# Optimization experiments

Measured on AMD Instinct MI355X. Metric: run time of the kernel, lower is better.

Reference implementation:

```python
import jax, jax.numpy as jnp
import numpy as np

N = 100000      # nodes
E = 1600000     # edges
G = 256         # graphs in the batch
D_IN = 128
H = 128
C = 10
EPS = 1e-5      # BatchNorm eps


def setup_inputs() -> dict:
    key = jax.random.key(0)
    ks = jax.random.split(key, 32)
    inp = {
        'x': jax.random.normal(ks[0], (N, D_IN), jnp.float32),
        'edge_index': jax.random.randint(ks[1], (2, E), 0, N, dtype=jnp.int64),
        'batch': jnp.sort(jax.random.randint(ks[2], (N,), 0, G, dtype=jnp.int64)),
        'w1': jax.random.normal(ks[3], (D_IN, H), jnp.float32) * 0.05,
        'b1': jax.random.normal(ks[4], (H,), jnp.float32) * 0.05,
        'w2': jax.random.normal(ks[5], (H, H), jnp.float32) * 0.05,
        'b2': jax.random.normal(ks[6], (H,), jnp.float32) * 0.05,
        'w3': jax.random.normal(ks[7], (H, H), jnp.float32) * 0.05,
        'b3': jax.random.normal(ks[8], (H,), jnp.float32) * 0.05,
        'g1': jax.random.uniform(ks[9], (H,), jnp.float32, 0.5, 1.5),
        'be1': jax.random.normal(ks[10], (H,), jnp.float32) * 0.05,
        'm1': jax.random.normal(ks[11], (H,), jnp.float32) * 0.05,
        'v1': jax.random.uniform(ks[12], (H,), jnp.float32, 0.5, 1.5),
        'g2': jax.random.uniform(ks[13], (H,), jnp.float32, 0.5, 1.5),
        'be2': jax.random.normal(ks[14], (H,), jnp.float32) * 0.05,
        'm2': jax.random.normal(ks[15], (H,), jnp.float32) * 0.05,
        'v2': jax.random.uniform(ks[16], (H,), jnp.float32, 0.5, 1.5),
        'g3': jax.random.uniform(ks[17], (H,), jnp.float32, 0.5, 1.5),
        'be3': jax.random.normal(ks[18], (H,), jnp.float32) * 0.05,
        'm3': jax.random.normal(ks[19], (H,), jnp.float32) * 0.05,
        'v3': jax.random.uniform(ks[20], (H,), jnp.float32, 0.5, 1.5),
        'fcw1': jax.random.normal(ks[21], (H, H // 2), jnp.float32) * 0.05,
        'fcb1': jax.random.normal(ks[22], (H // 2,), jnp.float32) * 0.05,
        'fcw2': jax.random.normal(ks[23], (H // 2, C), jnp.float32) * 0.05,
        'fcb2': jax.random.normal(ks[24], (C,), jnp.float32) * 0.05,
    }
    return inp


def _gcn_norm(edge_index, n_nodes):
    # add self loops (PyG GCNConv default) and compute D^-1/2 (A+I) D^-1/2 norms
    loop = jnp.arange(n_nodes, dtype=edge_index.dtype)
    src = jnp.concatenate([edge_index[0], loop])
    dst = jnp.concatenate([edge_index[1], loop])
    deg = jax.ops.segment_sum(jnp.ones_like(dst, dtype=jnp.float32), dst, num_segments=n_nodes)
    dinv = jnp.where(deg > 0, jax.lax.rsqrt(deg), 0.0)
    norm = dinv[src] * dinv[dst]  # [E+N]
    return src, dst, norm


def _gcn_conv(x, W, b, src, dst, norm, n_nodes):
    h = x @ W                                   # [N, H]
    msg = norm[:, None] * h[src]                # gather + scale, [E+N, H]
    return jax.ops.segment_sum(msg, dst, num_segments=n_nodes) + b


def _bn_eval(x, gamma, beta, mean, var):
    return (x - mean) * jax.lax.rsqrt(var + EPS) * gamma + beta


def reference(x, edge_index, batch, w1, b1, w2, b2, w3, b3,
              g1, be1, m1, v1, g2, be2, m2, v2, g3, be3, m3, v3,
              fcw1, fcb1, fcw2, fcb2):
    n = x.shape[0]
    x = jnp.nan_to_num(x, nan=0.0, posinf=1e6, neginf=-1e6)
    src, dst, norm = _gcn_norm(edge_index, n)

    h = jax.nn.relu(_bn_eval(_gcn_conv(x, w1, b1, src, dst, norm, n), g1, be1, m1, v1))
    h = jax.nn.relu(_bn_eval(_gcn_conv(h, w2, b2, src, dst, norm, n), g2, be2, m2, v2))
    h = jax.nn.relu(_bn_eval(_gcn_conv(h, w3, b3, src, dst, norm, n), g3, be3, m3, v3))

    # global_mean_pool over graphs
    sums = jax.ops.segment_sum(h, batch, num_segments=G)            # [G, H]
    cnts = jax.ops.segment_sum(jnp.ones((n,), h.dtype), batch, num_segments=G)
    pooled = sums / jnp.maximum(cnts, 1.0)[:, None]

    out = jax.nn.relu(pooled @ fcw1 + fcb1) @ fcw2 + fcb2           # [G, C]
    return out
```

## Files before the change

### kernel.cpp

```cpp
#include <hip/hip_runtime.h>
#include <math.h>

#define NN 100000
#define EE 1600000
#define GG 256
#define HH 128
#define BSH 8
#define NBK 391
#define PASSA_WG 391
#define CAPB 6144

typedef __attribute__((ext_vector_type(8))) short short8;
typedef __attribute__((ext_vector_type(4))) float f32x4;

union U4S8 { uint4 u; short8 s; };

static __device__ __forceinline__ unsigned bf16rne(float f) {
    const unsigned u = __float_as_uint(f);
    return (u + 0x7fffu + ((u >> 16) & 1u)) >> 16;
}
static __device__ __forceinline__ unsigned packbf(float a, float b) {
    return bf16rne(a) | (bf16rne(b) << 16);
}
static __device__ __forceinline__ float bflo(unsigned u) { return __uint_as_float(u << 16); }
static __device__ __forceinline__ float bfhi(unsigned u) { return __uint_as_float(u & 0xffff0000u); }

__global__ __launch_bounds__(256) void setup_k(
    const int* __restrict__ ei, const int* __restrict__ batch,
    const float* __restrict__ w1, const float* __restrict__ w2,
    const float* __restrict__ w3,
    const float* __restrict__ b1, const float* __restrict__ g1,
    const float* __restrict__ be1, const float* __restrict__ m1,
    const float* __restrict__ v1,
    const float* __restrict__ b2, const float* __restrict__ g2,
    const float* __restrict__ be2, const float* __restrict__ m2,
    const float* __restrict__ v2,
    const float* __restrict__ b3, const float* __restrict__ g3,
    const float* __restrict__ be3, const float* __restrict__ m3,
    const float* __restrict__ v3,
    unsigned* __restrict__ bt, float* __restrict__ sc, float* __restrict__ sh,
    int* __restrict__ cursor, float* __restrict__ psum, int* __restrict__ gcnt,
    int* __restrict__ flags) {
    const int id = blockIdx.x * 256 + threadIdx.x;
    if (id < 24576) {
        const int w = id >> 13;
        const int rem = id & 8191;
        const int n = rem >> 6;
        const int kk = rem & 63;
        const float* W = (w == 0) ? w1 : (w == 1) ? w2 : w3;
        bt[id] = packbf(W[(2 * kk) * HH + n], W[(2 * kk + 1) * HH + n]);
    } else if (id < 24704) {
        const int c = id - 24576;
        float s;
        s = g1[c] / sqrtf(v1[c] + 1e-5f);
        sc[c] = s;           sh[c] = (b1[c] - m1[c]) * s + be1[c];
        s = g2[c] / sqrtf(v2[c] + 1e-5f);
        sc[128 + c] = s;     sh[128 + c] = (b2[c] - m2[c]) * s + be2[c];
        s = g3[c] / sqrtf(v3[c] + 1e-5f);
        sc[256 + c] = s;     sh[256 + c] = (b3[c] - m3[c]) * s + be3[c];
    } else if (id < 25095) {
        const int b = id - 24704;
        cursor[b] = b * CAPB;
    } else if (id < 57863) {
        psum[id - 25095] = 0.0f;
    } else if (id < 58119) {
        gcnt[id - 57863] = 0;
    } else if (id == 58119) {
        int e64 = 1;
        for (int j = 0; j < 8; ++j) {
            if (ei[2 * EE - 1 - 2 * j] != 0) { e64 = 0; break; }
        }
        flags[0] = e64;
        flags[1] = (batch[NN - 1] == 0) ? 1 : 0;
    }
}
#define SETUP_GRID 228

__global__ __launch_bounds__(256) void passA_k(const int* __restrict__ ei,
                                               const int* __restrict__ flags,
                                               int* __restrict__ cursor,
                                               unsigned* __restrict__ pairs) {
    __shared__ int h[NBK];
    __shared__ int rbase[NBK];
    const int tid = threadIdx.x;
    for (int i = tid; i < NBK; i += 256) h[i] = 0;
    __syncthreads();
    const bool e64 = flags[0] != 0;
    const int base = blockIdx.x * 4096;
    int scache[16], dcache[16];
#pragma unroll
    for (int j = 0; j < 16; ++j) {
        const int e = base + j * 256 + tid;
        int s = -1, d = 0;
        if (e < EE) {
            s = e64 ? ei[2 * e] : ei[e];
            d = e64 ? ei[2 * (EE + e)] : ei[EE + e];
            atomicAdd(&h[d >> BSH], 1);
        }
        scache[j] = s; dcache[j] = d;
    }
    __syncthreads();
    for (int i = tid; i < NBK; i += 256) {
        const int c = h[i];
        rbase[i] = c ? atomicAdd(&cursor[i], c) : 0;
    }
    __syncthreads();
    for (int i = tid; i < NBK; i += 256) h[i] = 0;
    __syncthreads();
#pragma unroll
    for (int j = 0; j < 16; ++j) {
        const int s = scache[j];
        if (s >= 0) {
            const int d = dcache[j];
            const int b = d >> BSH;
            const int r = atomicAdd(&h[b], 1);
            pairs[rbase[b] + r] = ((unsigned)(d & 255) << 17) | (unsigned)s;
        }
    }
}

__global__ __launch_bounds__(256) void passB_k(const unsigned* __restrict__ pairs,
                                               const int* __restrict__ cursor,
                                               int* __restrict__ offs,
                                               int* __restrict__ degcnt,
                                               float* __restrict__ dinv,
                                               int* __restrict__ csr) {
    __shared__ unsigned pk[CAPB];
    __shared__ int cnt[256];
    __shared__ int loff[256];
    __shared__ int sc[256];
    const int tid = threadIdx.x;
    const int b = blockIdx.x;
    const int p0 = b * CAPB;
    const int np = cursor[b] - p0;
    const int nb0 = b << BSH;
    const int nnode = (NN - nb0 < 256) ? (NN - nb0) : 256;

    cnt[tid] = 0;
    __syncthreads();
    for (int i = tid; i < np; i += 256) {
        const unsigned p = pairs[p0 + i];
        pk[i] = p;
        atomicAdd(&cnt[p >> 17], 1);
    }
    __syncthreads();
    const int creal = cnt[tid];
    const int cpad = (tid < nnode) ? ((creal + 8) & ~7) : 0;
    sc[tid] = cpad;
    __syncthreads();
    for (int off = 1; off < 256; off <<= 1) {
        int t = (tid >= off) ? sc[tid - off] : 0;
        __syncthreads();
        sc[tid] += t;
        __syncthreads();
    }
    const int ex = sc[tid] - cpad;
    loff[tid] = ex;
    if (tid < nnode) {
        const int node = nb0 + tid;
        offs[node] = p0 + ex;
        degcnt[node] = creal;
        dinv[node] = 1.0f / sqrtf((float)(creal + 1));
    }
    __syncthreads();
    cnt[tid] = 0;
    __syncthreads();
    for (int i = tid; i < np; i += 256) {
        const unsigned p = pk[i];
        const int dl = (int)(p >> 17);
        const int r = atomicAdd(&cnt[dl], 1);
        csr[p0 + loff[dl] + r] = (int)(p & 0x1FFFFu);
    }
    if (tid < nnode) {
        const int basep = p0 + loff[tid];
        csr[basep + creal] = nb0 + tid;
        for (int j = creal + 1; j < cpad; ++j) csr[basep + j] = NN;
    }
}

static __device__ __forceinline__ float sani(float v) {
    if (isnan(v)) return 0.0f;
    if (isinf(v)) return v > 0.0f ? 1e6f : -1e6f;
    return v;
}

__global__ __launch_bounds__(256) void gemm_mfma_k(const float* __restrict__ Af,
                                                   const unsigned* __restrict__ btg,
                                                   const float* __restrict__ dinv,
                                                   unsigned* __restrict__ C, int M) {
    __shared__ unsigned lds_u[8704];
    const int tid = threadIdx.x;
    const int wave = tid >> 6;
    const int lane = tid & 63;
    const int nl = lane & 15;
    const int q = lane >> 4;
    const int row0 = blockIdx.x * 64 + wave * 16;
    const int rowg = row0 + nl;
    const int rowa = min(rowg, M - 1);

    {
        const uint4* __restrict__ bg4 = (const uint4*)btg;
        for (int i = tid; i < 2048; i += 256) {
            const int n = i >> 4, w4 = i & 15;
            *(uint4*)&lds_u[n * 68 + w4 * 4] = bg4[n * 16 + w4];
        }
    }

    short8 a[4];
#pragma unroll
    for (int ks = 0; ks < 4; ++ks) {
        const float4 p = *(const float4*)(Af + (size_t)rowa * HH + ks * 32 + q * 8);
        const float4 r = *(const float4*)(Af + (size_t)rowa * HH + ks * 32 + q * 8 + 4);
        U4S8 cv;
        cv.u = make_uint4(packbf(sani(p.x), sani(p.y)), packbf(sani(p.z), sani(p.w)),
                          packbf(sani(r.x), sani(r.y)), packbf(sani(r.z), sani(r.w)));
        a[ks] = cv.s;
    }

    __syncthreads();

    f32x4 acc[8];
#pragma unroll
    for (int t = 0; t < 8; ++t) acc[t] = (f32x4)0.0f;

    const unsigned short* __restrict__ bts = (const unsigned short*)lds_u;
#pragma unroll
    for (int ks = 0; ks < 4; ++ks) {
#pragma unroll
        for (int t = 0; t < 8; ++t) {
            const int n = t * 16 + nl;
            const short8 b = *(const short8*)(bts + n * 136 + ks * 32 + q * 8);
            acc[t] = __builtin_amdgcn_mfma_f32_16x16x32_bf16(b, a[ks], acc[t], 0, 0, 0);
        }
    }

    if (rowg < M) {
        const float dsc = dinv[rowg];
        unsigned* crow = C + (size_t)rowg * 64;
#pragma unroll
        for (int t = 0; t < 8; ++t) {
            uint2 o;
            o.x = packbf(dsc * acc[t][0], dsc * acc[t][1]);
            o.y = packbf(dsc * acc[t][2], dsc * acc[t][3]);
            *(uint2*)(crow + t * 8 + q * 2) = o;
        }
    } else if (rowg == M) {
        unsigned* crow = C + (size_t)M * 64;
#pragma unroll
        for (int t = 0; t < 8; ++t)
            *(uint2*)(crow + t * 8 + q * 2) = make_uint2(0u, 0u);
    }
}

__global__ __launch_bounds__(256) void agg_gemm_k(
    const unsigned* __restrict__ hin, const int* __restrict__ csr,
    const int* __restrict__ offs, const int* __restrict__ cnt,
    const float* __restrict__ dinv,
    const float* __restrict__ bnsc, const float* __restrict__ bnsh,
    const unsigned* __restrict__ btg,
    unsigned* __restrict__ hout) {
    __shared__ unsigned ybuf[16 * 68];
    const int tid = threadIdx.x;
    const int wave = tid >> 6;
    const int lane = tid & 63;
    const int cg = lane & 15;
    const int sub = lane >> 4;
    const int c8 = cg * 8;
    const char* __restrict__ hb = (const char*)hin;
    const unsigned cgo = (unsigned)(cg << 4);

    if (blockIdx.x == 0 && tid < 64) hout[(size_t)NN * 64 + tid] = 0u;

    const float4 sca = *(const float4*)(bnsc + c8);
    const float4 scb = *(const float4*)(bnsc + c8 + 4);
    const float4 sha = *(const float4*)(bnsh + c8);
    const float4 shb = *(const float4*)(bnsh + c8 + 4);

    for (int i = 0; i < 4; ++i) {
        const int v = __builtin_amdgcn_readfirstlane(blockIdx.x * 16 + wave * 4 + i);
        const float dv = dinv[v];
        const int start = offs[v];
        const int npad = (cnt[v] + 8) & ~7;

        float acc[8];
#pragma unroll
        for (int j = 0; j < 8; ++j) acc[j] = 0.0f;

        int e = 0;
        for (; e + 16 <= npad; e += 16) {
            const int sA = csr[start + e + sub];
            const int sB = csr[start + e + 4 + sub];
            const int sC = csr[start + e + 8 + sub];
            const int sD = csr[start + e + 12 + sub];
            const uint4 rA = *(const uint4*)(hb + (((unsigned)sA << 8) | cgo));
            const uint4 rB = *(const uint4*)(hb + (((unsigned)sB << 8) | cgo));
            const uint4 rC = *(const uint4*)(hb + (((unsigned)sC << 8) | cgo));
            const uint4 rD = *(const uint4*)(hb + (((unsigned)sD << 8) | cgo));
            acc[0] += (bflo(rA.x) + bflo(rB.x)) + (bflo(rC.x) + bflo(rD.x));
            acc[1] += (bfhi(rA.x) + bfhi(rB.x)) + (bfhi(rC.x) + bfhi(rD.x));
            acc[2] += (bflo(rA.y) + bflo(rB.y)) + (bflo(rC.y) + bflo(rD.y));
            acc[3] += (bfhi(rA.y) + bfhi(rB.y)) + (bfhi(rC.y) + bfhi(rD.y));
            acc[4] += (bflo(rA.z) + bflo(rB.z)) + (bflo(rC.z) + bflo(rD.z));
            acc[5] += (bfhi(rA.z) + bfhi(rB.z)) + (bfhi(rC.z) + bfhi(rD.z));
            acc[6] += (bflo(rA.w) + bflo(rB.w)) + (bflo(rC.w) + bflo(rD.w));
            acc[7] += (bfhi(rA.w) + bfhi(rB.w)) + (bfhi(rC.w) + bfhi(rD.w));
        }
        if (e < npad) {
            const int sA = csr[start + e + sub];
            const int sB = csr[start + e + 4 + sub];
            const uint4 rA = *(const uint4*)(hb + (((unsigned)sA << 8) | cgo));
            const uint4 rB = *(const uint4*)(hb + (((unsigned)sB << 8) | cgo));
            acc[0] += bflo(rA.x) + bflo(rB.x);
            acc[1] += bfhi(rA.x) + bfhi(rB.x);
            acc[2] += bflo(rA.y) + bflo(rB.y);
            acc[3] += bfhi(rA.y) + bfhi(rB.y);
            acc[4] += bflo(rA.z) + bflo(rB.z);
            acc[5] += bfhi(rA.z) + bfhi(rB.z);
            acc[6] += bflo(rA.w) + bflo(rB.w);
            acc[7] += bfhi(rA.w) + bfhi(rB.w);
        }

#pragma unroll
        for (int j = 0; j < 8; ++j) {
            acc[j] += __shfl_xor(acc[j], 16);
            acc[j] += __shfl_xor(acc[j], 32);
        }

        if (sub == 0) {
            const float y0 = fmaxf(dv * acc[0] * sca.x + sha.x, 0.0f);
            const float y1 = fmaxf(dv * acc[1] * sca.y + sha.y, 0.0f);
            const float y2 = fmaxf(dv * acc[2] * sca.z + sha.z, 0.0f);
            const float y3 = fmaxf(dv * acc[3] * sca.w + sha.w, 0.0f);
            const float y4 = fmaxf(dv * acc[4] * scb.x + shb.x, 0.0f);
            const float y5 = fmaxf(dv * acc[5] * scb.y + shb.y, 0.0f);
            const float y6 = fmaxf(dv * acc[6] * scb.z + shb.z, 0.0f);
            const float y7 = fmaxf(dv * acc[7] * scb.w + shb.w, 0.0f);
            *(uint4*)&ybuf[(wave * 4 + i) * 68 + cg * 4] =
                make_uint4(packbf(y0, y1), packbf(y2, y3), packbf(y4, y5), packbf(y6, y7));
        }
    }
    __syncthreads();

    const int nl = cg;
    const int q = sub;
    short8 arow[4];
#pragma unroll
    for (int ks = 0; ks < 4; ++ks) {
        U4S8 cv;
        cv.u = *(const uint4*)&ybuf[nl * 68 + ks * 16 + q * 4];
        arow[ks] = cv.s;
    }
    const uint4* __restrict__ bt4 = (const uint4*)btg;
    const int t0 = wave * 2;
    f32x4 acc0 = (f32x4)0.0f, acc1 = (f32x4)0.0f;
#pragma unroll
    for (int ks = 0; ks < 4; ++ks) {
        U4S8 b0, b1;
        b0.u = bt4[((t0 + 0) * 16 + nl) * 16 + ks * 4 + q];
        b1.u = bt4[((t0 + 1) * 16 + nl) * 16 + ks * 4 + q];
        acc0 = __builtin_amdgcn_mfma_f32_16x16x32_bf16(b0.s, arow[ks], acc0, 0, 0, 0);
        acc1 = __builtin_amdgcn_mfma_f32_16x16x32_bf16(b1.s, arow[ks], acc1, 0, 0, 0);
    }
    const int rowg = blockIdx.x * 16 + nl;
    const float dsc = dinv[rowg];
    unsigned* crow = hout + (size_t)rowg * 64;
    uint2 o0, o1;
    o0.x = packbf(dsc * acc0[0], dsc * acc0[1]);
    o0.y = packbf(dsc * acc0[2], dsc * acc0[3]);
    o1.x = packbf(dsc * acc1[0], dsc * acc1[1]);
    o1.y = packbf(dsc * acc1[2], dsc * acc1[3]);
    *(uint2*)(crow + (t0 + 0) * 8 + q * 2) = o0;
    *(uint2*)(crow + (t0 + 1) * 8 + q * 2) = o1;
}

__global__ __launch_bounds__(256) void aggregate_k(
    const unsigned* __restrict__ hpre, const int* __restrict__ csr,
    const int* __restrict__ offs, const int* __restrict__ cnt,
    const float* __restrict__ dinv,
    const float* __restrict__ bnsc, const float* __restrict__ bnsh,
    unsigned* __restrict__ xout) {
    const int v = __builtin_amdgcn_readfirstlane(blockIdx.x * 4 + (threadIdx.x >> 6));
    const int lane = threadIdx.x & 63;
    const int cg = lane & 15;
    const int sub = lane >> 4;
    const int c8 = cg * 8;

    const float dv = dinv[v];
    const int start = offs[v];
    const int npad = (cnt[v] + 8) & ~7;
    const char* __restrict__ hb = (const char*)hpre;
    const unsigned cgo = (unsigned)(cg << 4);

    float acc[8];
#pragma unroll
    for (int j = 0; j < 8; ++j) acc[j] = 0.0f;

    int i = 0;
    for (; i + 16 <= npad; i += 16) {
        const int sA = csr[start + i + sub];
        const int sB = csr[start + i + 4 + sub];
        const int sC = csr[start + i + 8 + sub];
        const int sD = csr[start + i + 12 + sub];
        const uint4 rA = *(const uint4*)(hb + (((unsigned)sA << 8) | cgo));
        const uint4 rB = *(const uint4*)(hb + (((unsigned)sB << 8) | cgo));
        const uint4 rC = *(const uint4*)(hb + (((unsigned)sC << 8) | cgo));
        const uint4 rD = *(const uint4*)(hb + (((unsigned)sD << 8) | cgo));
        acc[0] += (bflo(rA.x) + bflo(rB.x)) + (bflo(rC.x) + bflo(rD.x));
        acc[1] += (bfhi(rA.x) + bfhi(rB.x)) + (bfhi(rC.x) + bfhi(rD.x));
        acc[2] += (bflo(rA.y) + bflo(rB.y)) + (bflo(rC.y) + bflo(rD.y));
        acc[3] += (bfhi(rA.y) + bfhi(rB.y)) + (bfhi(rC.y) + bfhi(rD.y));
        acc[4] += (bflo(rA.z) + bflo(rB.z)) + (bflo(rC.z) + bflo(rD.z));
        acc[5] += (bfhi(rA.z) + bfhi(rB.z)) + (bfhi(rC.z) + bfhi(rD.z));
        acc[6] += (bflo(rA.w) + bflo(rB.w)) + (bflo(rC.w) + bflo(rD.w));
        acc[7] += (bfhi(rA.w) + bfhi(rB.w)) + (bfhi(rC.w) + bfhi(rD.w));
    }
    if (i < npad) {
        const int sA = csr[start + i + sub];
        const int sB = csr[start + i + 4 + sub];
        const uint4 rA = *(const uint4*)(hb + (((unsigned)sA << 8) | cgo));
        const uint4 rB = *(const uint4*)(hb + (((unsigned)sB << 8) | cgo));
        acc[0] += bflo(rA.x) + bflo(rB.x);
        acc[1] += bfhi(rA.x) + bfhi(rB.x);
        acc[2] += bflo(rA.y) + bflo(rB.y);
        acc[3] += bfhi(rA.y) + bfhi(rB.y);
        acc[4] += bflo(rA.z) + bflo(rB.z);
        acc[5] += bfhi(rA.z) + bfhi(rB.z);
        acc[6] += bflo(rA.w) + bflo(rB.w);
        acc[7] += bfhi(rA.w) + bfhi(rB.w);
    }

#pragma unroll
    for (int j = 0; j < 8; ++j) {
        acc[j] += __shfl_xor(acc[j], 16);
        acc[j] += __shfl_xor(acc[j], 32);
    }

    if (sub == 0) {
        const float4 sca = *(const float4*)(bnsc + c8);
        const float4 scb = *(const float4*)(bnsc + c8 + 4);
        const float4 sha = *(const float4*)(bnsh + c8);
        const float4 shb = *(const float4*)(bnsh + c8 + 4);
        const float y0 = fmaxf(dv * acc[0] * sca.x + sha.x, 0.0f);
        const float y1 = fmaxf(dv * acc[1] * sca.y + sha.y, 0.0f);
        const float y2 = fmaxf(dv * acc[2] * sca.z + sha.z, 0.0f);
        const float y3 = fmaxf(dv * acc[3] * sca.w + sha.w, 0.0f);
        const float y4 = fmaxf(dv * acc[4] * scb.x + shb.x, 0.0f);
        const float y5 = fmaxf(dv * acc[5] * scb.y + shb.y, 0.0f);
        const float y6 = fmaxf(dv * acc[6] * scb.z + shb.z, 0.0f);
        const float y7 = fmaxf(dv * acc[7] * scb.w + shb.w, 0.0f);
        *(uint4*)(xout + (size_t)v * 64 + cg * 4) =
            make_uint4(packbf(y0, y1), packbf(y2, y3), packbf(y4, y5), packbf(y6, y7));
    }
}

__global__ __launch_bounds__(256) void pool_sum_k(
    const unsigned* __restrict__ x, const int* __restrict__ batch,
    const int* __restrict__ flags, float* __restrict__ psum,
    int* __restrict__ gcnt) {
    const int wave = threadIdx.x >> 6;
    const int lane = threadIdx.x & 63;
    const int row0 = blockIdx.x * 64 + wave * 16;
    if (row0 >= NN) return;
    const bool b64 = flags[1] != 0;

    float sx = 0.0f, sy = 0.0f;
    int cur = -1, runlen = 0;
#pragma unroll
    for (int r = 0; r < 16; ++r) {
        const int row = row0 + r;
        if (row >= NN) break;
        const int g = b64 ? batch[2 * row] : batch[row];
        if (g != cur) {
            if (cur >= 0) {
                atomicAdd(&psum[cur * HH + lane * 2 + 0], sx);
                atomicAdd(&psum[cur * HH + lane * 2 + 1], sy);
                if (lane == 0) atomicAdd(&gcnt[cur], runlen);
            }
            cur = g; sx = 0.0f; sy = 0.0f; runlen = 0;
        }
        const unsigned u = x[(size_t)row * 64 + lane];
        sx += bflo(u);
        sy += bfhi(u);
        ++runlen;
    }
    if (cur >= 0) {
        atomicAdd(&psum[cur * HH + lane * 2 + 0], sx);
        atomicAdd(&psum[cur * HH + lane * 2 + 1], sy);
        if (lane == 0) atomicAdd(&gcnt[cur], runlen);
    }
}

__global__ __launch_bounds__(128) void head_k(
    const float* __restrict__ psum, const int* __restrict__ gcnt,
    const float* __restrict__ fw1, const float* __restrict__ fb1,
    const float* __restrict__ fw2, const float* __restrict__ fb2,
    float* __restrict__ out) {
    __shared__ float pooled[128];
    __shared__ float hid[64];
    const int g = blockIdx.x;
    const int tid = threadIdx.x;

    const int cntn = gcnt[g];
    pooled[tid] = psum[g * HH + tid] / (float)(cntn > 0 ? cntn : 1);
    __syncthreads();

    if (tid < 64) {
        float a = fb1[tid];
#pragma unroll 4
        for (int k = 0; k < 128; ++k) a += pooled[k] * fw1[k * 64 + tid];
        hid[tid] = fmaxf(a, 0.0f);
    }
    __syncthreads();
    if (tid < 10) {
        float a = fb2[tid];
#pragma unroll
        for (int k = 0; k < 64; ++k) a += hid[k] * fw2[k * 10 + tid];
        out[g * 10 + tid] = a;
    }
}

extern "C" void kernel_launch(void* const* d_in, const int* in_sizes, int n_in,
                              void* d_out, int out_size, void* d_ws, size_t ws_size,
                              hipStream_t stream) {
    const float* x_in  = (const float*)d_in[0];
    const int*   ei    = (const int*)d_in[1];
    const int*   batch = (const int*)d_in[2];
    const float* w1 = (const float*)d_in[3];
    const float* b1 = (const float*)d_in[4];
    const float* w2 = (const float*)d_in[5];
    const float* b2 = (const float*)d_in[6];
    const float* w3 = (const float*)d_in[7];
    const float* b3 = (const float*)d_in[8];
    const float* g1 = (const float*)d_in[9];
    const float* be1 = (const float*)d_in[10];
    const float* m1 = (const float*)d_in[11];
    const float* v1 = (const float*)d_in[12];
    const float* g2 = (const float*)d_in[13];
    const float* be2 = (const float*)d_in[14];
    const float* m2 = (const float*)d_in[15];
    const float* v2 = (const float*)d_in[16];
    const float* g3 = (const float*)d_in[17];
    const float* be3 = (const float*)d_in[18];
    const float* m3 = (const float*)d_in[19];
    const float* v3 = (const float*)d_in[20];
    const float* fw1 = (const float*)d_in[21];
    const float* fb1 = (const float*)d_in[22];
    const float* fw2 = (const float*)d_in[23];
    const float* fb2 = (const float*)d_in[24];
    float* out = (float*)d_out;

    size_t off = 0;
    char* base = (char*)d_ws;
    auto alloc = [&](size_t bytes) -> void* {
        void* p = base + off;
        off += (bytes + 255) & ~(size_t)255;
        return p;
    };
    int*      degcnt = (int*)alloc((size_t)NN * 4);
    float*    dinv   = (float*)alloc((size_t)NN * 4);
    int*      offs   = (int*)alloc((size_t)NN * 4);
    int*      cursor = (int*)alloc((size_t)NBK * 4);
    int*      flags  = (int*)alloc(256);
    float*    bnsc   = (float*)alloc(3 * 128 * 4);
    float*    bnsh   = (float*)alloc(3 * 128 * 4);
    unsigned* btg    = (unsigned*)alloc(3 * 8192 * 4);
    float*    psum   = (float*)alloc((size_t)GG * HH * 4);
    int*      gcnt   = (int*)alloc((size_t)GG * 4);
    int*      csr    = (int*)alloc((size_t)NBK * CAPB * 4);
    unsigned* pairs  = (unsigned*)alloc((size_t)NBK * CAPB * 4);
    unsigned* bufA   = (unsigned*)alloc((size_t)(NN + 1) * 64 * 4);
    unsigned* bufB   = (unsigned*)alloc((size_t)(NN + 1) * 64 * 4);
    if (off > ws_size) return;

    setup_k<<<SETUP_GRID, 256, 0, stream>>>(ei, batch, w1, w2, w3,
                                            b1, g1, be1, m1, v1,
                                            b2, g2, be2, m2, v2,
                                            b3, g3, be3, m3, v3,
                                            btg, bnsc, bnsh, cursor, psum, gcnt,
                                            flags);
    passA_k<<<PASSA_WG, 256, 0, stream>>>(ei, flags, cursor, pairs);
    passB_k<<<NBK, 256, 0, stream>>>(pairs, cursor, offs, degcnt, dinv, csr);

    const int ggrid = (NN + 63) / 64;
    const int fgrid = NN / 16;
    const int agrid = NN / 4;

    gemm_mfma_k<<<ggrid, 256, 0, stream>>>(x_in, btg, dinv, bufA, NN);
    agg_gemm_k<<<fgrid, 256, 0, stream>>>(bufA, csr, offs, degcnt, dinv,
                                          bnsc, bnsh, btg + 8192, bufB);
    agg_gemm_k<<<fgrid, 256, 0, stream>>>(bufB, csr, offs, degcnt, dinv,
                                          bnsc + 128, bnsh + 128, btg + 16384, bufA);
    aggregate_k<<<agrid, 256, 0, stream>>>(bufA, csr, offs, degcnt, dinv,
                                           bnsc + 256, bnsh + 256, bufB);

    pool_sum_k<<<ggrid, 256, 0, stream>>>(bufB, batch, flags, psum, gcnt);
    head_k<<<GG, 128, 0, stream>>>(psum, gcnt, fw1, fb1, fw2, fb2, out);
}
```

Baseline: 440.7 us.

## Interleave four-node gathers and fuse final aggregation with mean-pool accumulation

Adds a gather4 helper in which each wave gathers neighbour rows for four nodes at once, prefetching the next CSR indices while the current loads are in flight, and padding idle nodes with the zero row. Both agg_gemm_k and a new agg_pool_k use it. The last aggregate and pool kernels are fused: the layer-3 activations stay in shared memory and are reduced per graph with atomics, so the bf16 intermediate is never written and re-read. The cost is more registers for the four accumulator sets, and wasted loads when the four nodes differ widely in degree.

```diff
diff --git a/kernel.cpp b/kernel.cpp
--- a/kernel.cpp
+++ b/kernel.cpp
@@ -252,6 +252,47 @@
     }
 }
 
+static __device__ __forceinline__ void gather4(
+    const char* __restrict__ hb, const int* __restrict__ csr,
+    const int st[4], const int np[4], const int maxp,
+    const int sub, const unsigned cgo, float acc[4][8]) {
+    int ia[4], ib[4];
+#pragma unroll
+    for (int i = 0; i < 4; ++i) {
+        ia[i] = csr[st[i] + sub];
+        ib[i] = csr[st[i] + 4 + sub];
+    }
+    for (int e = 0; e < maxp; e += 8) {
+        uint4 r[8];
+#pragma unroll
+        for (int i = 0; i < 4; ++i) {
+            const bool act = (e < np[i]);
+            const unsigned sA = act ? (unsigned)ia[i] : (unsigned)NN;
+            const unsigned sB = act ? (unsigned)ib[i] : (unsigned)NN;
+            r[2 * i]     = *(const uint4*)(hb + ((sA << 8) | cgo));
+            r[2 * i + 1] = *(const uint4*)(hb + ((sB << 8) | cgo));
+        }
+#pragma unroll
+        for (int i = 0; i < 4; ++i) {
+            ia[i] = csr[st[i] + e + 8 + sub];
+            ib[i] = csr[st[i] + e + 12 + sub];
+        }
+#pragma unroll
+        for (int i = 0; i < 4; ++i) {
+            const uint4 rA = r[2 * i];
+            const uint4 rB = r[2 * i + 1];
+            acc[i][0] += bflo(rA.x) + bflo(rB.x);
+            acc[i][1] += bfhi(rA.x) + bfhi(rB.x);
+            acc[i][2] += bflo(rA.y) + bflo(rB.y);
+            acc[i][3] += bfhi(rA.y) + bfhi(rB.y);
+            acc[i][4] += bflo(rA.z) + bflo(rB.z);
+            acc[i][5] += bfhi(rA.z) + bfhi(rB.z);
+            acc[i][6] += bflo(rA.w) + bflo(rB.w);
+            acc[i][7] += bfhi(rA.w) + bfhi(rB.w);
+        }
+    }
+}
+
 __global__ __launch_bounds__(256) void agg_gemm_k(
     const unsigned* __restrict__ hin, const int* __restrict__ csr,
     const int* __restrict__ offs, const int* __restrict__ cnt,
@@ -271,70 +312,47 @@
 
     if (blockIdx.x == 0 && tid < 64) hout[(size_t)NN * 64 + tid] = 0u;
 
+    int st[4], np[4];
+    float dvv[4];
+#pragma unroll
+    for (int i = 0; i < 4; ++i) {
+        const int v = __builtin_amdgcn_readfirstlane(blockIdx.x * 16 + wave * 4 + i);
+        st[i] = offs[v];
+        np[i] = (cnt[v] + 8) & ~7;
+        dvv[i] = dinv[v];
+    }
+    const int maxp = max(max(np[0], np[1]), max(np[2], np[3]));
+
+    float acc[4][8];
+#pragma unroll
+    for (int i = 0; i < 4; ++i)
+#pragma unroll
+        for (int j = 0; j < 8; ++j) acc[i][j] = 0.0f;
+
+    gather4(hb, csr, st, np, maxp, sub, cgo, acc);
+
     const float4 sca = *(const float4*)(bnsc + c8);
     const float4 scb = *(const float4*)(bnsc + c8 + 4);
     const float4 sha = *(const float4*)(bnsh + c8);
     const float4 shb = *(const float4*)(bnsh + c8 + 4);
 
+#pragma unroll
     for (int i = 0; i < 4; ++i) {
-        const int v = __builtin_amdgcn_readfirstlane(blockIdx.x * 16 + wave * 4 + i);
-        const float dv = dinv[v];
-        const int start = offs[v];
-        const int npad = (cnt[v] + 8) & ~7;
-
-        float acc[8];
-#pragma unroll
-        for (int j = 0; j < 8; ++j) acc[j] = 0.0f;
-
-        int e = 0;
-        for (; e + 16 <= npad; e += 16) {
-            const int sA = csr[start + e + sub];
-            const int sB = csr[start + e + 4 + sub];
-            const int sC = csr[start + e + 8 + sub];
-            const int sD = csr[start + e + 12 + sub];
-            const uint4 rA = *(const uint4*)(hb + (((unsigned)sA << 8) | cgo));
-            const uint4 rB = *(const uint4*)(hb + (((unsigned)sB << 8) | cgo));
-            const uint4 rC = *(const uint4*)(hb + (((unsigned)sC << 8) | cgo));
-            const uint4 rD = *(const uint4*)(hb + (((unsigned)sD << 8) | cgo));
-            acc[0] += (bflo(rA.x) + bflo(rB.x)) + (bflo(rC.x) + bflo(rD.x));
-            acc[1] += (bfhi(rA.x) + bfhi(rB.x)) + (bfhi(rC.x) + bfhi(rD.x));
-            acc[2] += (bflo(rA.y) + bflo(rB.y)) + (bflo(rC.y) + bflo(rD.y));
-            acc[3] += (bfhi(rA.y) + bfhi(rB.y)) + (bfhi(rC.y) + bfhi(rD.y));
-            acc[4] += (bflo(rA.z) + bflo(rB.z)) + (bflo(rC.z) + bflo(rD.z));
-            acc[5] += (bfhi(rA.z) + bfhi(rB.z)) + (bfhi(rC.z) + bfhi(rD.z));
-            acc[6] += (bflo(rA.w) + bflo(rB.w)) + (bflo(rC.w) + bflo(rD.w));
-            acc[7] += (bfhi(rA.w) + bfhi(rB.w)) + (bfhi(rC.w) + bfhi(rD.w));
-        }
-        if (e < npad) {
-            const int sA = csr[start + e + sub];
-            const int sB = csr[start + e + 4 + sub];
-            const uint4 rA = *(const uint4*)(hb + (((unsigned)sA << 8) | cgo));
-            const uint4 rB = *(const uint4*)(hb + (((unsigned)sB << 8) | cgo));
-            acc[0] += bflo(rA.x) + bflo(rB.x);
-            acc[1] += bfhi(rA.x) + bfhi(rB.x);
-            acc[2] += bflo(rA.y) + bflo(rB.y);
-            acc[3] += bfhi(rA.y) + bfhi(rB.y);
-            acc[4] += bflo(rA.z) + bflo(rB.z);
-            acc[5] += bfhi(rA.z) + bfhi(rB.z);
-            acc[6] += bflo(rA.w) + bflo(rB.w);
-            acc[7] += bfhi(rA.w) + bfhi(rB.w);
-        }
-
 #pragma unroll
         for (int j = 0; j < 8; ++j) {
-            acc[j] += __shfl_xor(acc[j], 16);
-            acc[j] += __shfl_xor(acc[j], 32);
-        }
-
+            acc[i][j] += __shfl_xor(acc[i][j], 16);
+            acc[i][j] += __shfl_xor(acc[i][j], 32);
+        }
         if (sub == 0) {
-            const float y0 = fmaxf(dv * acc[0] * sca.x + sha.x, 0.0f);
-            const float y1 = fmaxf(dv * acc[1] * sca.y + sha.y, 0.0f);
-            const float y2 = fmaxf(dv * acc[2] * sca.z + sha.z, 0.0f);
-            const float y3 = fmaxf(dv * acc[3] * sca.w + sha.w, 0.0f);
-            const float y4 = fmaxf(dv * acc[4] * scb.x + shb.x, 0.0f);
-            const float y5 = fmaxf(dv * acc[5] * scb.y + shb.y, 0.0f);
-            const float y6 = fmaxf(dv * acc[6] * scb.z + shb.z, 0.0f);
-            const float y7 = fmaxf(dv * acc[7] * scb.w + shb.w, 0.0f);
+            const float dv = dvv[i];
+            const float y0 = fmaxf(dv * acc[i][0] * sca.x + sha.x, 0.0f);
+            const float y1 = fmaxf(dv * acc[i][1] * sca.y + sha.y, 0.0f);
+            const float y2 = fmaxf(dv * acc[i][2] * sca.z + sha.z, 0.0f);
+            const float y3 = fmaxf(dv * acc[i][3] * sca.w + sha.w, 0.0f);
+            const float y4 = fmaxf(dv * acc[i][4] * scb.x + shb.x, 0.0f);
+            const float y5 = fmaxf(dv * acc[i][5] * scb.y + shb.y, 0.0f);
+            const float y6 = fmaxf(dv * acc[i][6] * scb.z + shb.z, 0.0f);
+            const float y7 = fmaxf(dv * acc[i][7] * scb.w + shb.w, 0.0f);
             *(uint4*)&ybuf[(wave * 4 + i) * 68 + cg * 4] =
                 make_uint4(packbf(y0, y1), packbf(y2, y3), packbf(y4, y5), packbf(y6, y7));
         }
@@ -373,120 +391,95 @@
     *(uint2*)(crow + (t0 + 1) * 8 + q * 2) = o1;
 }
 
-__global__ __launch_bounds__(256) void aggregate_k(
+__global__ __launch_bounds__(256) void agg_pool_k(
     const unsigned* __restrict__ hpre, const int* __restrict__ csr,
     const int* __restrict__ offs, const int* __restrict__ cnt,
     const float* __restrict__ dinv,
     const float* __restrict__ bnsc, const float* __restrict__ bnsh,
-    unsigned* __restrict__ xout) {
-    const int v = __builtin_amdgcn_readfirstlane(blockIdx.x * 4 + (threadIdx.x >> 6));
-    const int lane = threadIdx.x & 63;
+    const int* __restrict__ batch, const int* __restrict__ flags,
+    float* __restrict__ psum, int* __restrict__ gcnt) {
+    __shared__ float yb[16][128];
+    __shared__ int gid[16];
+    const int tid = threadIdx.x;
+    const int wave = tid >> 6;
+    const int lane = tid & 63;
     const int cg = lane & 15;
     const int sub = lane >> 4;
     const int c8 = cg * 8;
-
-    const float dv = dinv[v];
-    const int start = offs[v];
-    const int npad = (cnt[v] + 8) & ~7;
     const char* __restrict__ hb = (const char*)hpre;
     const unsigned cgo = (unsigned)(cg << 4);
-
-    float acc[8];
-#pragma unroll
-    for (int j = 0; j < 8; ++j) acc[j] = 0.0f;
-
-    int i = 0;
-    for (; i + 16 <= npad; i += 16) {
-        const int sA = csr[start + i + sub];
-        const int sB = csr[start + i + 4 + sub];
-        const int sC = csr[start + i + 8 + sub];
-        const int sD = csr[start + i + 12 + sub];
-        const uint4 rA = *(const uint4*)(hb + (((unsigned)sA << 8) | cgo));
-        const uint4 rB = *(const uint4*)(hb + (((unsigned)sB << 8) | cgo));
-        const uint4 rC = *(const uint4*)(hb + (((unsigned)sC << 8) | cgo));
-        const uint4 rD = *(const uint4*)(hb + (((unsigned)sD << 8) | cgo));
-        acc[0] += (bflo(rA.x) + bflo(rB.x)) + (bflo(rC.x) + bflo(rD.x));
-        acc[1] += (bfhi(rA.x) + bfhi(rB.x)) + (bfhi(rC.x) + bfhi(rD.x));
-        acc[2] += (bflo(rA.y) + bflo(rB.y)) + (bflo(rC.y) + bflo(rD.y));
-        acc[3] += (bfhi(rA.y) + bfhi(rB.y)) + (bfhi(rC.y) + bfhi(rD.y));
-        acc[4] += (bflo(rA.z) + bflo(rB.z)) + (bflo(rC.z) + bflo(rD.z));
-        acc[5] += (bfhi(rA.z) + bfhi(rB.z)) + (bfhi(rC.z) + bfhi(rD.z));
-        acc[6] += (bflo(rA.w) + bflo(rB.w)) + (bflo(rC.w) + bflo(rD.w));
-        acc[7] += (bfhi(rA.w) + bfhi(rB.w)) + (bfhi(rC.w) + bfhi(rD.w));
-    }
-    if (i < npad) {
-        const int sA = csr[start + i + sub];
-        const int sB = csr[start + i + 4 + sub];
-        const uint4 rA = *(const uint4*)(hb + (((unsigned)sA << 8) | cgo));
-        const uint4 rB = *(const uint4*)(hb + (((unsigned)sB << 8) | cgo));
-        acc[0] += bflo(rA.x) + bflo(rB.x);
-        acc[1] += bfhi(rA.x) + bfhi(rB.x);
-        acc[2] += bflo(rA.y) + bflo(rB.y);
-        acc[3] += bfhi(rA.y) + bfhi(rB.y);
-        acc[4] += bflo(rA.z) + bflo(rB.z);
-        acc[5] += bfhi(rA.z) + bfhi(rB.z);
-        acc[6] += bflo(rA.w) + bflo(rB.w);
-        acc[7] += bfhi(rA.w) + bfhi(rB.w);
-    }
-
-#pragma unroll
-    for (int j = 0; j < 8; ++j) {
-        acc[j] += __shfl_xor(acc[j], 16);
-        acc[j] += __shfl_xor(acc[j], 32);
-    }
-
-    if (sub == 0) {
-        const float4 sca = *(const float4*)(bnsc + c8);
-        const float4 scb = *(const float4*)(bnsc + c8 + 4);
-        const float4 sha = *(const float4*)(bnsh + c8);
-        const float4 shb = *(const float4*)(bnsh + c8 + 4);
-        const float y0 = fmaxf(dv * acc[0] * sca.x + sha.x, 0.0f);
-        const float y1 = fmaxf(dv * acc[1] * sca.y + sha.y, 0.0f);
-        const float y2 = fmaxf(dv * acc[2] * sca.z + sha.z, 0.0f);
-        const float y3 = fmaxf(dv * acc[3] * sca.w + sha.w, 0.0f);
-        const float y4 = fmaxf(dv * acc[4] * scb.x + shb.x, 0.0f);
-        const float y5 = fmaxf(dv * acc[5] * scb.y + shb.y, 0.0f);
-        const float y6 = fmaxf(dv * acc[6] * scb.z + shb.z, 0.0f);
-        const float y7 = fmaxf(dv * acc[7] * scb.w + shb.w, 0.0f);
-        *(uint4*)(xout + (size_t)v * 64 + cg * 4) =
-            make_uint4(packbf(y0, y1), packbf(y2, y3), packbf(y4, y5), packbf(y6, y7));
-    }
-}
-
-__global__ __launch_bounds__(256) void pool_sum_k(
-    const unsigned* __restrict__ x, const int* __restrict__ batch,
-    const int* __restrict__ flags, float* __restrict__ psum,
-    int* __restrict__ gcnt) {
-    const int wave = threadIdx.x >> 6;
-    const int lane = threadIdx.x & 63;
-    const int row0 = blockIdx.x * 64 + wave * 16;
-    if (row0 >= NN) return;
     const bool b64 = flags[1] != 0;
 
-    float sx = 0.0f, sy = 0.0f;
-    int cur = -1, runlen = 0;
-#pragma unroll
-    for (int r = 0; r < 16; ++r) {
-        const int row = row0 + r;
-        if (row >= NN) break;
-        const int g = b64 ? batch[2 * row] : batch[row];
-        if (g != cur) {
-            if (cur >= 0) {
-                atomicAdd(&psum[cur * HH + lane * 2 + 0], sx);
-                atomicAdd(&psum[cur * HH + lane * 2 + 1], sy);
-                if (lane == 0) atomicAdd(&gcnt[cur], runlen);
+    int st[4], np[4];
+    float dvv[4];
+#pragma unroll
+    for (int i = 0; i < 4; ++i) {
+        const int v = __builtin_amdgcn_readfirstlane(blockIdx.x * 16 + wave * 4 + i);
+        st[i] = offs[v];
+        np[i] = (cnt[v] + 8) & ~7;
+        dvv[i] = dinv[v];
+        if (lane == 0) gid[wave * 4 + i] = b64 ? batch[2 * v] : batch[v];
+    }
+    const int maxp = max(max(np[0], np[1]), max(np[2], np[3]));
+
+    float acc[4][8];
+#pragma unroll
+    for (int i = 0; i < 4; ++i)
+#pragma unroll
+        for (int j = 0; j < 8; ++j) acc[i][j] = 0.0f;
+
+    gather4(hb, csr, st, np, maxp, sub, cgo, acc);
+
+    const float4 sca = *(const float4*)(bnsc + c8);
+    const float4 scb = *(const float4*)(bnsc + c8 + 4);
+    const float4 sha = *(const float4*)(bnsh + c8);
+    const float4 shb = *(const float4*)(bnsh + c8 + 4);
+
+#pragma unroll
+    for (int i = 0; i < 4; ++i) {
+#pragma unroll
+        for (int j = 0; j < 8; ++j) {
+            acc[i][j] += __shfl_xor(acc[i][j], 16);
+            acc[i][j] += __shfl_xor(acc[i][j], 32);
+        }
+        if (sub == 0) {
+            const float dv = dvv[i];
+            const int row = wave * 4 + i;
+            yb[row][c8 + 0] = fmaxf(dv * acc[i][0] * sca.x + sha.x, 0.0f);
+            yb[row][c8 + 1] = fmaxf(dv * acc[i][1] * sca.y + sha.y, 0.0f);
+            yb[row][c8 + 2] = fmaxf(dv * acc[i][2] * sca.z + sha.z, 0.0f);
+            yb[row][c8 + 3] = fmaxf(dv * acc[i][3] * sca.w + sha.w, 0.0f);
+            yb[row][c8 + 4] = fmaxf(dv * acc[i][4] * scb.x + shb.x, 0.0f);
+            yb[row][c8 + 5] = fmaxf(dv * acc[i][5] * scb.y + shb.y, 0.0f);
+            yb[row][c8 + 6] = fmaxf(dv * acc[i][6] * scb.z + shb.z, 0.0f);
+            yb[row][c8 + 7] = fmaxf(dv * acc[i][7] * scb.w + shb.w, 0.0f);
+        }
+    }
+    __syncthreads();
+
+    if (tid < 128) {
+        float s = 0.0f;
+        int cur = gid[0];
+        for (int r = 0; r < 16; ++r) {
+            const int g = gid[r];
+            if (g != cur) {
+                atomicAdd(&psum[cur * HH + tid], s);
+                cur = g; s = 0.0f;
             }
-            cur = g; sx = 0.0f; sy = 0.0f; runlen = 0;
-        }
-        const unsigned u = x[(size_t)row * 64 + lane];
-        sx += bflo(u);
-        sy += bfhi(u);
-        ++runlen;
-    }
-    if (cur >= 0) {
-        atomicAdd(&psum[cur * HH + lane * 2 + 0], sx);
-        atomicAdd(&psum[cur * HH + lane * 2 + 1], sy);
-        if (lane == 0) atomicAdd(&gcnt[cur], runlen);
+            s += yb[r][tid];
+        }
+        atomicAdd(&psum[cur * HH + tid], s);
+    } else if (tid == 128) {
+        int cur = gid[0], c = 0;
+        for (int r = 0; r < 16; ++r) {
+            const int g = gid[r];
+            if (g != cur) {
+                atomicAdd(&gcnt[cur], c);
+                cur = g; c = 0;
+            }
+            ++c;
+        }
+        atomicAdd(&gcnt[cur], c);
     }
 }
 
@@ -583,16 +576,14 @@
 
     const int ggrid = (NN + 63) / 64;
     const int fgrid = NN / 16;
-    const int agrid = NN / 4;
 
     gemm_mfma_k<<<ggrid, 256, 0, stream>>>(x_in, btg, dinv, bufA, NN);
     agg_gemm_k<<<fgrid, 256, 0, stream>>>(bufA, csr, offs, degcnt, dinv,
                                           bnsc, bnsh, btg + 8192, bufB);
     agg_gemm_k<<<fgrid, 256, 0, stream>>>(bufB, csr, offs, degcnt, dinv,
                                           bnsc + 128, bnsh + 128, btg + 16384, bufA);
-    aggregate_k<<<agrid, 256, 0, stream>>>(bufA, csr, offs, degcnt, dinv,
-                                           bnsc + 256, bnsh + 256, bufB);
-
-    pool_sum_k<<<ggrid, 256, 0, stream>>>(bufB, batch, flags, psum, gcnt);
+    agg_pool_k<<<fgrid, 256, 0, stream>>>(bufA, csr, offs, degcnt, dinv,
+                                          bnsc + 256, bnsh + 256, batch, flags,
+                                          psum, gcnt);
     head_k<<<GG, 128, 0, stream>>>(psum, gcnt, fw1, fb1, fw2, fb2, out);
 }
```

Measured after the change: 408.9 us. -7.2%, faster.
